# Performance work log

Measured on AMD Instinct MI355X. Metric: run time of the kernel, lower is better.

The kernel has to match this reference:

```python
import jax, jax.numpy as jnp
import numpy as np

N_NODES = 50000
N_EDGES = 1_600_000
IN_DIM = 128
OUT_DIM = 128


def setup_inputs() -> dict:
    key = jax.random.key(0)
    k1, k2, k3, k4, k5, k6 = jax.random.split(key, 6)
    H = jax.random.normal(k1, (N_NODES, IN_DIM), dtype=jnp.float32)
    edge_src = jax.random.randint(k2, (N_EDGES,), 0, N_NODES, dtype=jnp.int32)
    edge_dst = jnp.sort(jax.random.randint(k3, (N_EDGES,), 0, N_NODES, dtype=jnp.int32))
    edge_weight = jax.random.uniform(k4, (N_EDGES,), dtype=jnp.float32)
    bound = np.sqrt(6.0 / (IN_DIM + OUT_DIM))
    W = jax.random.uniform(k5, (IN_DIM, OUT_DIM), dtype=jnp.float32, minval=-bound, maxval=bound)
    b = jax.random.normal(k6, (OUT_DIM,), dtype=jnp.float32)
    return {"H": H, "edge_src": edge_src, "edge_dst": edge_dst,
            "edge_weight": edge_weight, "W": W, "b": b}


def reference(H, edge_src, edge_dst, edge_weight, W, b):
    # A_hat @ H: gather source features, scale by edge weight, scatter-sum to dst.
    msgs = edge_weight[:, None] * jnp.take(H, edge_src, axis=0)   # [E, in_dim]
    agg = jax.ops.segment_sum(msgs, edge_dst, num_segments=N_NODES)  # [N, in_dim]
    # Dense transform + bias (no activation in original forward).
    return agg @ W + b
```

## Files before the change

### kernel.cpp

```cpp
#include <hip/hip_runtime.h>

#define IN_DIM 128
#define OUT_DIM 128

typedef __attribute__((ext_vector_type(8))) short short8v;
typedef __attribute__((ext_vector_type(4))) float float4v;
typedef __attribute__((ext_vector_type(4))) unsigned int uint4v;

__device__ __forceinline__ ushort f2bf(float f) {
    unsigned int u = __builtin_bit_cast(unsigned int, f);
    unsigned int r = (u + 0x7fffu + ((u >> 16) & 1u)) >> 16;
    return (ushort)r;
}

__device__ __forceinline__ unsigned int pk2bf(float x, float y) {
#if __has_builtin(__builtin_amdgcn_cvt_pk_bf16_f32)
    typedef __attribute__((ext_vector_type(2))) __bf16 bf2;
    bf2 r = __builtin_amdgcn_cvt_pk_bf16_f32(x, y);
    return __builtin_bit_cast(unsigned int, r);
#else
    return (unsigned int)f2bf(x) | ((unsigned int)f2bf(y) << 16);
#endif
}

__global__ __launch_bounds__(256) void prep_kernel(const float* __restrict__ W,
                                                   ushort* __restrict__ Wt) {
    int k0 = blockIdx.x * 8;
    int n = threadIdx.x & 127;
    int half = threadIdx.x >> 7;
#pragma unroll
    for (int kp = 0; kp < 2; ++kp) {
        int k = k0 + (half * 2 + kp) * 2;
        float v0 = W[k * 128 + n];
        float v1 = W[(k + 1) * 128 + n];
        *(unsigned int*)&Wt[n * 136 + k] = pk2bf(v0, v1);
    }
}

__global__ __launch_bounds__(256) void gemm_kernel(const float* __restrict__ H,
                                                   const ushort* __restrict__ Wt_g,
                                                   unsigned char* __restrict__ T8,
                                                   float* __restrict__ S, int M,
                                                   const int* __restrict__ edst,
                                                   int* __restrict__ rp,
                                                   int E, int nb_gemm) {
    __shared__ ushort Ws[128 * 136];

    const int t = threadIdx.x;

    if (blockIdx.x >= nb_gemm) {
        int n = (blockIdx.x - nb_gemm) * 256 + t;
        if (n <= M) {
            int lo = 0, hi = E;
            while (lo < hi) {
                int mid = (lo + hi) >> 1;
                if (edst[mid] < n) lo = mid + 1; else hi = mid;
            }
            rp[n] = lo;
        }
        return;
    }

    const int row0 = blockIdx.x * 64;

#pragma unroll
    for (int f = t; f < 2176; f += 256)
        ((short8v*)Ws)[f] = ((const short8v*)Wt_g)[f];

    const int w = t >> 6;
    const int l = t & 63;
    const int m16 = l & 15;
    const int kq = (l >> 4) * 8;
    const int gr = row0 + w * 16 + m16;

    float4 h[8];
    if (gr < M) {
#pragma unroll
        for (int ks = 0; ks < 4; ++ks) {
            h[ks * 2]     = *(const float4*)&H[gr * 128 + ks * 32 + kq];
            h[ks * 2 + 1] = *(const float4*)&H[gr * 128 + ks * 32 + kq + 4];
        }
    } else {
#pragma unroll
        for (int i = 0; i < 8; ++i) h[i] = make_float4(0.f, 0.f, 0.f, 0.f);
    }

    short8v bfrag[4];
#pragma unroll
    for (int ks = 0; ks < 4; ++ks) {
        uint4v u;
        u[0] = pk2bf(h[ks * 2].x, h[ks * 2].y);
        u[1] = pk2bf(h[ks * 2].z, h[ks * 2].w);
        u[2] = pk2bf(h[ks * 2 + 1].x, h[ks * 2 + 1].y);
        u[3] = pk2bf(h[ks * 2 + 1].z, h[ks * 2 + 1].w);
        bfrag[ks] = __builtin_bit_cast(short8v, u);
    }

    __syncthreads();

    float4v acc[8];
#pragma unroll
    for (int nt = 0; nt < 8; ++nt) acc[nt] = (float4v){0.f, 0.f, 0.f, 0.f};

#pragma unroll
    for (int ks = 0; ks < 4; ++ks) {
#pragma unroll
        for (int nt = 0; nt < 8; ++nt) {
            short8v afrag = *(const short8v*)&Ws[(nt * 16 + m16) * 136 + ks * 32 + kq];
            acc[nt] = __builtin_amdgcn_mfma_f32_16x16x32_bf16(afrag, bfrag[ks], acc[nt], 0, 0, 0);
        }
    }

    float mx = 0.f;
#pragma unroll
    for (int nt = 0; nt < 8; ++nt) {
#pragma unroll
        for (int k = 0; k < 4; ++k) mx = fmaxf(mx, fabsf(acc[nt][k]));
    }
    mx = fmaxf(mx, __shfl_xor(mx, 16));
    mx = fmaxf(mx, __shfl_xor(mx, 32));

    const float inv = 127.0f / fmaxf(mx, 1e-20f);

    if (gr < M) {
        const int qd = l >> 4;
        if (qd == 0) S[gr] = mx * (1.0f / 127.0f);
#pragma unroll
        for (int nt = 0; nt < 8; ++nt) {
            unsigned int p = 0;
#pragma unroll
            for (int k = 0; k < 4; ++k) {
                int qi = (int)__builtin_rintf(acc[nt][k] * inv);
                qi = qi > 127 ? 127 : (qi < -127 ? -127 : qi);
                p |= ((unsigned int)(qi + 128) & 0xffu) << (k * 8);
            }
            *(unsigned int*)&T8[gr * 128 + nt * 16 + qd * 4] = p;
        }
    }
}

__global__ __launch_bounds__(256) void scatter_kernel(const unsigned char* __restrict__ T8,
                                                      const float* __restrict__ S,
                                                      const int* __restrict__ esrc,
                                                      const float* __restrict__ ew,
                                                      const int* __restrict__ rp,
                                                      const float* __restrict__ b,
                                                      float* __restrict__ out) {
    const int node = blockIdx.x * 4 + (threadIdx.x >> 6);
    const int lane = threadIdx.x & 63;
    const int half = lane >> 5;
    const unsigned int colb = (lane & 31u) * 4u;

    const int s = __builtin_amdgcn_readfirstlane(rp[node]);
    const int e = __builtin_amdgcn_readfirstlane(rp[node + 1]);

    float ax0 = 0.f, ax1 = 0.f, ax2 = 0.f, ax3 = 0.f;
    float B = 0.f;

    for (int c = s; c < e; c += 64) {
        const int idx = c + lane;
        int srcl = 0;
        float wl = 0.f;
        if (idx < e) { srcl = esrc[idx]; wl = ew[idx]; }
        const float wsl = wl * S[srcl];
        int nn = e - c;
        if (nn > 64) nn = 64;

        for (int j = 0; j < nn; j += 8) {
            int sqp[4];
            float wsp[4];
            unsigned int vv[4];
#pragma unroll
            for (int p = 0; p < 4; ++p) {
                const int srcLane = j + p * 2 + half;
                sqp[p] = __shfl(srcl, srcLane);
                wsp[p] = __shfl(wsl, srcLane);
            }
#pragma unroll
            for (int p = 0; p < 4; ++p)
                vv[p] = *(const unsigned int*)(T8 + ((unsigned int)sqp[p] * 128u + colb));
#pragma unroll
            for (int p = 0; p < 4; ++p) {
                const unsigned int v = vv[p];
                const float ws = wsp[p];
                B += ws;
                ax0 = fmaf((float)(v & 0xffu), ws, ax0);
                ax1 = fmaf((float)((v >> 8) & 0xffu), ws, ax1);
                ax2 = fmaf((float)((v >> 16) & 0xffu), ws, ax2);
                ax3 = fmaf((float)(v >> 24), ws, ax3);
            }
        }
    }

    ax0 += __shfl_xor(ax0, 32);
    ax1 += __shfl_xor(ax1, 32);
    ax2 += __shfl_xor(ax2, 32);
    ax3 += __shfl_xor(ax3, 32);
    B   += __shfl_xor(B, 32);

    if (half == 0) {
        const float4 bb = *(const float4*)&b[colb];
        float4 o;
        o.x = fmaf(-128.0f, B, ax0) + bb.x;
        o.y = fmaf(-128.0f, B, ax1) + bb.y;
        o.z = fmaf(-128.0f, B, ax2) + bb.z;
        o.w = fmaf(-128.0f, B, ax3) + bb.w;
        *(float4*)&out[node * 128 + colb] = o;
    }
}

extern "C" void kernel_launch(void* const* d_in, const int* in_sizes, int n_in,
                              void* d_out, int out_size, void* d_ws, size_t ws_size,
                              hipStream_t stream) {
    const float* H    = (const float*)d_in[0];
    const int*   esrc = (const int*)d_in[1];
    const int*   edst = (const int*)d_in[2];
    const float* ew   = (const float*)d_in[3];
    const float* W    = (const float*)d_in[4];
    const float* b    = (const float*)d_in[5];
    float* out = (float*)d_out;

    const int M = in_sizes[0] / IN_DIM;
    const int E = in_sizes[1];

    unsigned char* T8 = (unsigned char*)d_ws;
    size_t off = (size_t)M * 128;
    float* S  = (float*)((char*)d_ws + off);
    off += (size_t)M * 4;
    ushort* Wt = (ushort*)((char*)d_ws + off);
    off += 128 * 136 * 2;
    int* rp = (int*)((char*)d_ws + off);

    prep_kernel<<<16, 256, 0, stream>>>(W, Wt);

    const int nb_gemm = (M + 63) / 64;
    const int nb_rp   = (M + 1 + 255) / 256;
    gemm_kernel<<<nb_gemm + nb_rp, 256, 0, stream>>>(H, Wt, T8, S, M, edst, rp, E, nb_gemm);

    scatter_kernel<<<(M + 3) / 4, 256, 0, stream>>>(T8, S, esrc, ew, rp, b, out);
}
```

Baseline: 132.9 us.

## Split scatter columns across two blocks with four edges per wave step

The scatter kernel now assigns each node's 128 output columns to two separate blocks, each covering 64 columns. Within a wave, four quarters of 16 lanes each handle a different edge, instead of two halves over the full row. Block indices are interleaved so the two column halves of the same node group run close together in time. This doubles the number of blocks and halves the bytes per gathered row segment, which raises memory-level parallelism. The cost is that edge indices, weights and row pointers are read twice and each reduction needs an extra shuffle stage.

Result: slower. 147.9 us (+11.3%).

```diff
diff --git a/kernel.cpp b/kernel.cpp
--- a/kernel.cpp
+++ b/kernel.cpp
@@ -145,16 +145,23 @@
                                                       const float* __restrict__ ew,
                                                       const int* __restrict__ rp,
                                                       const float* __restrict__ b,
-                                                      float* __restrict__ out) {
-    const int node = blockIdx.x * 4 + (threadIdx.x >> 6);
+                                                      float* __restrict__ out,
+                                                      int M, int ngroups) {
+    const int blk = blockIdx.x;
+    const int halfsel = (blk & 7) >> 2;
+    const int i = ((blk >> 3) << 2) + (blk & 3);
+    if (i >= ngroups) return;
+    const int node = i * 4 + (threadIdx.x >> 6);
+    if (node >= M) return;
+
     const int lane = threadIdx.x & 63;
-    const int half = lane >> 5;
-    const unsigned int colb = (lane & 31u) * 4u;
+    const int quarter = lane >> 4;
+    const unsigned int colb = (unsigned int)halfsel * 64u + (lane & 15u) * 4u;
 
     const int s = __builtin_amdgcn_readfirstlane(rp[node]);
     const int e = __builtin_amdgcn_readfirstlane(rp[node + 1]);
 
-    float ax0 = 0.f, ax1 = 0.f, ax2 = 0.f, ax3 = 0.f;
+    float a0 = 0.f, a1 = 0.f, a2 = 0.f, a3 = 0.f;
     float B = 0.f;
 
     for (int c = s; c < e; c += 64) {
@@ -166,45 +173,45 @@
         int nn = e - c;
         if (nn > 64) nn = 64;
 
-        for (int j = 0; j < nn; j += 8) {
-            int sqp[4];
-            float wsp[4];
+        for (int j = 0; j < nn; j += 16) {
+            int sq[4];
+            float ws[4];
             unsigned int vv[4];
 #pragma unroll
             for (int p = 0; p < 4; ++p) {
-                const int srcLane = j + p * 2 + half;
-                sqp[p] = __shfl(srcl, srcLane);
-                wsp[p] = __shfl(wsl, srcLane);
+                const int sl = j + p * 4 + quarter;
+                sq[p] = __shfl(srcl, sl);
+                ws[p] = __shfl(wsl, sl);
             }
 #pragma unroll
             for (int p = 0; p < 4; ++p)
-                vv[p] = *(const unsigned int*)(T8 + ((unsigned int)sqp[p] * 128u + colb));
+                vv[p] = *(const unsigned int*)(T8 + ((unsigned int)sq[p] * 128u + colb));
 #pragma unroll
             for (int p = 0; p < 4; ++p) {
                 const unsigned int v = vv[p];
-                const float ws = wsp[p];
-                B += ws;
-                ax0 = fmaf((float)(v & 0xffu), ws, ax0);
-                ax1 = fmaf((float)((v >> 8) & 0xffu), ws, ax1);
-                ax2 = fmaf((float)((v >> 16) & 0xffu), ws, ax2);
-                ax3 = fmaf((float)(v >> 24), ws, ax3);
-            }
-        }
-    }
-
-    ax0 += __shfl_xor(ax0, 32);
-    ax1 += __shfl_xor(ax1, 32);
-    ax2 += __shfl_xor(ax2, 32);
-    ax3 += __shfl_xor(ax3, 32);
-    B   += __shfl_xor(B, 32);
-
-    if (half == 0) {
+                const float w = ws[p];
+                B  += w;
+                a0 = fmaf((float)(v & 0xffu), w, a0);
+                a1 = fmaf((float)((v >> 8) & 0xffu), w, a1);
+                a2 = fmaf((float)((v >> 16) & 0xffu), w, a2);
+                a3 = fmaf((float)(v >> 24), w, a3);
+            }
+        }
+    }
+
+    a0 += __shfl_xor(a0, 16); a0 += __shfl_xor(a0, 32);
+    a1 += __shfl_xor(a1, 16); a1 += __shfl_xor(a1, 32);
+    a2 += __shfl_xor(a2, 16); a2 += __shfl_xor(a2, 32);
+    a3 += __shfl_xor(a3, 16); a3 += __shfl_xor(a3, 32);
+    B  += __shfl_xor(B, 16);  B  += __shfl_xor(B, 32);
+
+    if (quarter == 0) {
         const float4 bb = *(const float4*)&b[colb];
         float4 o;
-        o.x = fmaf(-128.0f, B, ax0) + bb.x;
-        o.y = fmaf(-128.0f, B, ax1) + bb.y;
-        o.z = fmaf(-128.0f, B, ax2) + bb.z;
-        o.w = fmaf(-128.0f, B, ax3) + bb.w;
+        o.x = fmaf(-128.0f, B, a0) + bb.x;
+        o.y = fmaf(-128.0f, B, a1) + bb.y;
+        o.z = fmaf(-128.0f, B, a2) + bb.z;
+        o.w = fmaf(-128.0f, B, a3) + bb.w;
         *(float4*)&out[node * 128 + colb] = o;
     }
 }
@@ -237,5 +244,8 @@
     const int nb_rp   = (M + 1 + 255) / 256;
     gemm_kernel<<<nb_gemm + nb_rp, 256, 0, stream>>>(H, Wt, T8, S, M, edst, rp, E, nb_gemm);
 
-    scatter_kernel<<<(M + 3) / 4, 256, 0, stream>>>(T8, S, esrc, ew, rp, b, out);
-}
+    const int ngroups  = (M + 3) / 4;
+    const int ngroups4 = ((ngroups + 3) / 4) * 4;
+    const int nblk     = 2 * ngroups4;
+    scatter_kernel<<<nblk, 256, 0, stream>>>(T8, S, esrc, ew, rp, b, out, M, ngroups);
+}
```
